# Kernel tuning notes

Measured on AMD Instinct MI355X. Metric: run time of the kernel, lower is better.

## Reference

```python
import jax, jax.numpy as jnp
import numpy as np

N_HEADS = 16
NOPE = 128
ROPE = 64
VDIM = 128
HEAD_DIM = NOPE + ROPE  # 192


def apply_rope(x, cos, sin):
    # x: [B, S, H, D] with D even; pairs (a, b) rotated by complex freqs.
    B, S, H, D = x.shape
    xr = x.reshape(B, S, H, D // 2, 2)
    a, b = xr[..., 0], xr[..., 1]
    c = cos[None, :, None, :]
    s = sin[None, :, None, :]
    out = jnp.stack([a * c - b * s, a * s + b * c], axis=-1)
    return out.reshape(B, S, H, D)


def setup_inputs() -> dict:
    key = jax.random.key(0)
    ks = jax.random.split(key, 8)
    B, S, DIM = 1, 2048, 2048
    x = jax.random.normal(ks[0], (B, S, DIM), dtype=jnp.float32)
    wq = jax.random.normal(ks[1], (N_HEADS * HEAD_DIM, DIM), dtype=jnp.float32) * (DIM ** -0.5)
    wk = jax.random.normal(ks[2], (N_HEADS * HEAD_DIM, DIM), dtype=jnp.float32) * (DIM ** -0.5)
    wv = jax.random.normal(ks[3], (N_HEADS * VDIM, DIM), dtype=jnp.float32) * (DIM ** -0.5)
    wo = jax.random.normal(ks[4], (DIM, N_HEADS * VDIM), dtype=jnp.float32) * ((N_HEADS * VDIM) ** -0.5)
    # rotary freqs: theta = 10000^{-2i/d}, angles = pos * theta
    inv_freq = 1.0 / (10000.0 ** (np.arange(0, ROPE, 2, dtype=np.float32) / ROPE))
    angles = np.arange(S, dtype=np.float32)[:, None] * inv_freq[None, :]  # [S, 32]
    freqs_cos = jnp.asarray(np.cos(angles))
    freqs_sin = jnp.asarray(np.sin(angles))
    # additive causal mask
    mask = jnp.where(jnp.triu(jnp.ones((S, S), dtype=bool), k=1), -1e9, 0.0).astype(jnp.float32)
    return {"x": x, "wq": wq, "wk": wk, "wv": wv, "wo": wo,
            "freqs_cos": freqs_cos, "freqs_sin": freqs_sin, "mask": mask, "start_pos": 0}


def reference(x, wq, wk, wv, wo, freqs_cos, freqs_sin, mask, start_pos):
    B, S, DIM = x.shape
    q = (x @ wq.T).reshape(B, S, N_HEADS, HEAD_DIM)
    k = (x @ wk.T).reshape(B, S, N_HEADS, HEAD_DIM)
    v = (x @ wv.T).reshape(B, S, N_HEADS, VDIM)
    q_nope, q_pe = q[..., :NOPE], q[..., NOPE:]
    k_nope, k_pe = k[..., :NOPE], k[..., NOPE:]
    q_pe = apply_rope(q_pe, freqs_cos, freqs_sin)
    k_pe = apply_rope(k_pe, freqs_cos, freqs_sin)
    scores = (jnp.einsum('bshd,bthd->bsht', q_nope, k_nope)
              + jnp.einsum('bshd,bthd->bsht', q_pe, k_pe)) * (HEAD_DIM ** -0.5)
    scores = scores + mask[None, :, None, :]
    probs = jax.nn.softmax(scores.astype(jnp.float32), axis=-1).astype(x.dtype)
    out = jnp.einsum('bsht,bthd->bshd', probs, v)
    return out.reshape(B, S, N_HEADS * VDIM) @ wo.T
```

## Files before the change

### kernel.cpp

```cpp
#include <hip/hip_runtime.h>
#include <hip/hip_bf16.h>
#include <math.h>

#define NH 16
#define NOPE 128
#define ROPE 64
#define VDIM 128
#define HD 192
#define SEQ 2048
#define DIM 2048
#define QKD (NH * HD)
#define VD  (NH * VDIM)
#define QKVS 8192

typedef __attribute__((ext_vector_type(8))) short short8;
typedef __attribute__((ext_vector_type(4))) short short4v;
typedef __attribute__((ext_vector_type(4))) float f32x4;
typedef unsigned int u32;

#define WAIT_VM8  0x0F78
#define WAIT_VM6  0x0F76
#define WAIT_VM4  0x0F74
#define WAIT_VM3  0x0F73
#define WAIT_VM2  0x0F72
#define WAIT_VM0  0x0F70
#define WAIT_LGKM 0xC07F

static __device__ inline short f2bf(float f) {
  union { float f; unsigned u; } v; v.f = f;
  unsigned r = (v.u + 0x7fffu + ((v.u >> 16) & 1u)) >> 16;
  return (short)r;
}
static __device__ inline float bf2f(unsigned short u) {
  union { unsigned u; float f; } v; v.u = ((unsigned)u) << 16;
  return v.f;
}

static __device__ __forceinline__ void gload16(const short* g, short* l) {
  __builtin_amdgcn_global_load_lds(
      (const __attribute__((address_space(1))) u32*)g,
      (__attribute__((address_space(3))) u32*)l, 16, 0, 0);
}


#define LSA(pp) (Lsm + (pp) * 65536)
#define LSB(pp) (Lsm + (pp) * 65536 + 32768)

#define RDA(pp, kh, mh) do { \
  const char* p_ = LSA(pp) + abase + (mh) * 8192 + ((kh) ? cx1 : cx0); \
  afr[(mh) * 4 + 0] = *(const short8*)(p_ + 0); \
  afr[(mh) * 4 + 1] = *(const short8*)(p_ + 2048); \
  afr[(mh) * 4 + 2] = *(const short8*)(p_ + 4096); \
  afr[(mh) * 4 + 3] = *(const short8*)(p_ + 6144); \
} while (0)

#define RDB(pp, kh) do { \
  const char* p_ = LSB(pp) + bbase + ((kh) ? cx1 : cx0); \
  bfr[0] = *(const short8*)(p_ + 0); \
  bfr[1] = *(const short8*)(p_ + 2048); \
  bfr[2] = *(const short8*)(p_ + 4096); \
  bfr[3] = *(const short8*)(p_ + 6144); \
} while (0)

#define SGA(kt, c) gload16(srcA[c] + (kt) * 64, (short*)(LSA((kt) & 1) + ((c) * 512 + tid) * 16))
#define SGB(kt, c) gload16(srcB[c] + (kt) * 64, (short*)(LSB((kt) & 1) + ((c) * 512 + tid) * 16))
#define G1S(kt) do { SGA(kt, 0); SGA(kt, 2); SGB(kt, 0); SGB(kt, 1); } while (0)
#define G2S(kt) do { SGA(kt, 1); SGA(kt, 3); SGB(kt, 2); SGB(kt, 3); } while (0)

#define MFMA1(mi, ni) \
  acc[mi][ni] = __builtin_amdgcn_mfma_f32_16x16x32_bf16(afr[mi], bfr[ni], acc[mi][ni], 0, 0, 0)

#define MM(mh) do { \
  MFMA1((mh)*4+0, 0); MFMA1((mh)*4+1, 0); MFMA1((mh)*4+2, 0); MFMA1((mh)*4+3, 0); \
  MFMA1((mh)*4+0, 1); MFMA1((mh)*4+1, 1); MFMA1((mh)*4+2, 1); MFMA1((mh)*4+3, 1); \
  MFMA1((mh)*4+0, 2); MFMA1((mh)*4+1, 2); MFMA1((mh)*4+2, 2); MFMA1((mh)*4+3, 2); \
  MFMA1((mh)*4+0, 3); MFMA1((mh)*4+1, 3); MFMA1((mh)*4+2, 3); MFMA1((mh)*4+3, 3); \
} while (0)

#define GBAR() __builtin_amdgcn_s_barrier()
#define GLGKM0() __builtin_amdgcn_s_waitcnt(WAIT_LGKM)
#define GPRIO1() __builtin_amdgcn_s_setprio(1)
#define GPRIO0() __builtin_amdgcn_s_setprio(0)
#define GNOP ((void)0)

#define TILE(pp, SP1, SP4, VMW) do { \
  RDA(pp, 0, 0); RDB(pp, 0); SP1; \
  GBAR(); GLGKM0(); GPRIO1(); MM(0); GPRIO0(); GBAR(); \
  RDA(pp, 0, 1); \
  GBAR(); GLGKM0(); GPRIO1(); MM(1); GPRIO0(); GBAR(); \
  RDA(pp, 1, 0); RDB(pp, 1); \
  GBAR(); GLGKM0(); GPRIO1(); MM(0); GPRIO0(); GBAR(); \
  RDA(pp, 1, 1); SP4; \
  GBAR(); GLGKM0(); GPRIO1(); MM(1); GPRIO0(); VMW; GBAR(); \
} while (0)

__global__ __launch_bounds__(512, 2) void gemm256_bt(
    const short* __restrict__ A, const short* __restrict__ B,
    short* __restrict__ C, int K, int lda, int ldb, int ldc) {
  __shared__ __align__(16) char Lsm[131072];

  const int tid = threadIdx.x;
  const int lane = tid & 63;
  const int l15 = lane & 15;
  const int quad = lane >> 4;
  const int wv = tid >> 6;
  const int wr = wv >> 2, wc = wv & 3;

  const int bid = blockIdx.x;
  const int xcd = bid & 7;
  const int idx = bid >> 3;
  const int m0 = (idx & 7) * 256;
  const int n0 = (xcd * 4 + (idx >> 3)) * 256;

  const int trow = tid >> 3;
  const int scol = ((tid & 7) * 8) ^ ((trow & 7) * 8);
  const short* srcA[4]; const short* srcB[4];
#pragma unroll
  for (int c = 0; c < 4; ++c) {
    srcA[c] = A + (size_t)(m0 + c * 64 + trow) * lda + scol;
    srcB[c] = B + (size_t)(n0 + c * 64 + trow) * ldb + scol;
  }

  const int abase = (wr * 128 + l15) * 128;
  const int bbase = (wc * 64 + l15) * 128;
  const int cx0 = (quad * 16) ^ ((l15 & 7) * 16);
  const int cx1 = (64 + quad * 16) ^ ((l15 & 7) * 16);

  f32x4 acc[8][4];
#pragma unroll
  for (int i = 0; i < 8; ++i)
#pragma unroll
    for (int j = 0; j < 4; ++j) acc[i][j] = (f32x4)(0.f);
  short8 afr[8], bfr[4];

  const int NT = K >> 6;

  G1S(0); G2S(0); G1S(1);
  __builtin_amdgcn_s_waitcnt(WAIT_VM4);
  GBAR();

  int kt = 0;
  for (; kt + 4 <= NT; kt += 2) {
    TILE(0, G2S(kt + 1), G1S(kt + 2), __builtin_amdgcn_s_waitcnt(WAIT_VM4));
    TILE(1, G2S(kt + 2), G1S(kt + 3), __builtin_amdgcn_s_waitcnt(WAIT_VM4));
  }
  TILE(0, G2S(kt + 1), GNOP, __builtin_amdgcn_s_waitcnt(WAIT_VM0));
  TILE(1, GNOP, GNOP, GNOP);

#pragma unroll
  for (int m = 0; m < 8; ++m) {
    const size_t rb = (size_t)(m0 + wr * 128 + m * 16 + quad * 4) * ldc +
                      n0 + wc * 64 + l15;
#pragma unroll
    for (int n = 0; n < 4; ++n)
#pragma unroll
      for (int r = 0; r < 4; ++r)
        C[rb + (size_t)r * ldc + n * 16] = f2bf(acc[m][n][r]);
  }
}

template <bool BF16OUT>
__global__ __launch_bounds__(256) void gemm_bt(
    const short* __restrict__ A, const short* __restrict__ B,
    void* __restrict__ Cv, int K, int lda, int ldb, int ldc, float oscale) {
  __shared__ __align__(16) short Ls[4][2][4096];

  const int tid = threadIdx.x;
  const int lane = tid & 63;
  const int wave = tid >> 6;
  const int wr = wave >> 1, wc = wave & 1;
  const int lane15 = lane & 15, quad = lane >> 4;
  const int m0 = blockIdx.y * 128, n0 = blockIdx.x * 128;

  const short* gA[4]; const short* gB[4];
#pragma unroll
  for (int i = 0; i < 4; ++i) {
    int gidx = i * 64 + lane;
    int r = gidx >> 2, p = gidx & 3;
    int g = (p ^ ((r >> 1) & 3)) * 8;
    gA[i] = A + (size_t)(m0 + wr * 64 + r) * lda + g;
    gB[i] = B + (size_t)(n0 + wc * 64 + r) * ldb + g;
  }

  f32x4 acc[4][4];
#pragma unroll
  for (int i = 0; i < 4; ++i)
#pragma unroll
    for (int j = 0; j < 4; ++j) acc[i][j] = (f32x4)(0.f);

#pragma unroll
  for (int i = 0; i < 4; ++i) gload16(gA[i], &Ls[wave][0][i * 512]);
#pragma unroll
  for (int i = 0; i < 4; ++i) gload16(gB[i], &Ls[wave][0][2048 + i * 512]);

  const int rsw = (lane15 >> 1) & 3;
  for (int k0 = 0; k0 < K; k0 += 32) {
    const int cur = (k0 >> 5) & 1;
    __builtin_amdgcn_s_waitcnt(WAIT_LGKM);
    if (k0 + 32 < K) {
      const int nxt = cur ^ 1;
#pragma unroll
      for (int i = 0; i < 4; ++i) gload16(gA[i] + k0 + 32, &Ls[wave][nxt][i * 512]);
#pragma unroll
      for (int i = 0; i < 4; ++i) gload16(gB[i] + k0 + 32, &Ls[wave][nxt][2048 + i * 512]);
      __builtin_amdgcn_s_waitcnt(WAIT_VM8);
    } else {
      __builtin_amdgcn_s_waitcnt(WAIT_VM0);
    }
    const short* bufp = &Ls[wave][cur][0];
    short8 af[4], bfv[4];
#pragma unroll
    for (int i = 0; i < 4; ++i)
      af[i] = *(const short8*)&bufp[(i * 16 + lane15) * 32 + (quad ^ rsw) * 8];
#pragma unroll
    for (int j = 0; j < 4; ++j)
      bfv[j] = *(const short8*)&bufp[2048 + (j * 16 + lane15) * 32 + (quad ^ rsw) * 8];
#pragma unroll
    for (int i = 0; i < 4; ++i)
#pragma unroll
      for (int j = 0; j < 4; ++j)
        acc[i][j] = __builtin_amdgcn_mfma_f32_16x16x32_bf16(af[i], bfv[j], acc[i][j], 0, 0, 0);
  }

#pragma unroll
  for (int i = 0; i < 4; ++i)
#pragma unroll
    for (int j = 0; j < 4; ++j)
#pragma unroll
      for (int r = 0; r < 4; ++r) {
        size_t idx = (size_t)(m0 + wr * 64 + i * 16 + quad * 4 + r) * ldc +
                     n0 + wc * 64 + j * 16 + lane15;
        if (BF16OUT)
          ((short*)Cv)[idx] = f2bf(acc[i][j][r] * oscale);
        else
          ((float*)Cv)[idx] = acc[i][j][r];
      }
}

__global__ __launch_bounds__(256) void rope_qk(
    short* __restrict__ qk, const float* __restrict__ cosf, const float* __restrict__ sinf) {
  int idx = blockIdx.x * blockDim.x + threadIdx.x;
  int j = idx & 31;
  int h = (idx >> 5) & (NH - 1);
  int s = idx >> 9;
  if (s >= SEQ) return;

  float c = cosf[s * 32 + j];
  float sn = sinf[s * 32 + j];
  size_t rowb = (size_t)s * QKVS + h * HD + NOPE + 2 * j;

  u32* pq = (u32*)(qk + rowb);
  u32 w = *pq;
  float a = bf2f((unsigned short)(w & 0xffff));
  float b = bf2f((unsigned short)(w >> 16));
  *pq = (u32)(unsigned short)f2bf(a * c - b * sn) |
        ((u32)(unsigned short)f2bf(a * sn + b * c) << 16);

  u32* pk = (u32*)(qk + rowb + QKD);
  w = *pk;
  a = bf2f((unsigned short)(w & 0xffff));
  b = bf2f((unsigned short)(w >> 16));
  *pk = (u32)(unsigned short)f2bf(a * c - b * sn) |
        ((u32)(unsigned short)f2bf(a * sn + b * c) << 16);
}

__global__ __launch_bounds__(256) void conv_in(
    const float* __restrict__ x, const float* __restrict__ wq,
    const float* __restrict__ wk, const float* __restrict__ wv,
    short* __restrict__ xb, short* __restrict__ wqkv) {
  const int NX4v = DIM * DIM / 4;
  int i = blockIdx.x * 256 + threadIdx.x;
  float4 f; short* dst; int di;
  if (i < NX4v) {
    f = ((const float4*)x)[i]; dst = xb; di = i;
  } else {
    int j = i - NX4v;
    int row = j >> 9;
    if (row < QKD) f = ((const float4*)wq)[j];
    else if (row < 2 * QKD) f = ((const float4*)wk)[j - QKD * (DIM / 4)];
    else f = ((const float4*)wv)[j - 2 * QKD * (DIM / 4)];
    dst = wqkv; di = j;
  }
  short4v o;
  o.x = f2bf(f.x); o.y = f2bf(f.y); o.z = f2bf(f.z); o.w = f2bf(f.w);
  ((short4v*)dst)[di] = o;
}

__global__ __launch_bounds__(256) void bf16_convert(
    const float* __restrict__ in, short* __restrict__ out, int n4) {
  int i = blockIdx.x * 256 + threadIdx.x;
  if (i >= n4) return;
  float4 f = ((const float4*)in)[i];
  short4v o;
  o.x = f2bf(f.x); o.y = f2bf(f.y); o.z = f2bf(f.z); o.w = f2bf(f.w);
  ((short4v*)out)[i] = o;
}

__global__ __launch_bounds__(256) void vt_bf16(
    const short* __restrict__ vb, short* __restrict__ vtb) {
  __shared__ short tile[64][74];
  const int t0 = blockIdx.x * 64;
  const int c0 = blockIdx.y * 64;
  const int tid = threadIdx.x;
#pragma unroll
  for (int i = 0; i < 16; ++i) {
    int idx = i * 256 + tid;
    int r = idx >> 6, c = idx & 63;
    tile[r][c] = vb[(size_t)(t0 + r) * QKVS + c0 + c];
  }
  __syncthreads();
  const int h = c0 >> 7;
  const int dbase = c0 & 127;
#pragma unroll
  for (int i = 0; i < 16; ++i) {
    int idx = i * 256 + tid;
    int d = idx >> 6, t = idx & 63;
    vtb[(size_t)h * VDIM * SEQ + (size_t)(dbase + d) * SEQ + t0 + t] = tile[t][d];
  }
}

#define BQ 128
#define BT 64
#define CHT 8
#define PSTR2 36
#define MFIX 8.0f

__global__ __launch_bounds__(512, 4) void attn_part(
    const short* __restrict__ qk,
    const short* __restrict__ vtb,
    short* __restrict__ Opart,
    float* __restrict__ lpart)
{
  __shared__ __align__(16) short Ks[2][BT * 192];
  __shared__ __align__(16) short Vt[VDIM * BT];
  __shared__ __align__(16) short Ps[8 * 16 * PSTR2];

  const int xcd = blockIdx.x;
  const int i0 = blockIdx.y;
  const int h = xcd + ((i0 >= 40) ? 8 : 0);
  int jj = (i0 >= 40) ? (i0 - 40) : i0;
  int qtb = 15;
  while (jj >= (qtb >> 2) + 1) { jj -= (qtb >> 2) + 1; --qtb; }
  const int chk = jj;

  const int tid = threadIdx.x;
  const int wave = tid >> 6;
  const int lane = tid & 63;
  const int lane15 = lane & 15;
  const int quad = lane >> 4;
  const int g = qtb >> 2;
  const int slot = h * 40 + (g + 1) * (2 * g + (qtb & 3)) + chk;
  const int R0 = qtb * BQ;
  const int NT = 2 * qtb + 2;
  const int kt_beg = chk * CHT;
  const int kt_end = min(kt_beg + CHT, NT);
  const float scale = 0.072168784f;

  const int qrow = R0 + wave * 16 + lane15;
  short8 qf[6];
  const short* qbase = qk + (size_t)qrow * QKVS + h * HD + quad * 8;
#pragma unroll
  for (int kc = 0; kc < 6; ++kc) qf[kc] = *(const short8*)(qbase + kc * 32);
  __builtin_amdgcn_s_waitcnt(WAIT_VM0);
  __builtin_amdgcn_sched_barrier(0);

  const short* kb = qk + QKD;
  int lKoff[3]; const short* gK[3];
#pragma unroll
  for (int i = 0; i < 3; ++i) {
    int id = i * 512 + tid;
    int row = id / 24, cX = id - row * 24;
    int ch = cX ^ (row & 7);
    lKoff[i] = id * 8;
    gK[i] = kb + (size_t)row * QKVS + h * HD + ch * 8;
  }
  const short* gV[2]; short* lV[2];
#pragma unroll
  for (int i = 0; i < 2; ++i) {
    int id = i * 512 + tid;
    int row = id >> 3, cX = id & 7;
    int ch = cX ^ (row & 7);
    lV[i] = &Vt[id * 8];
    gV[i] = vtb + (size_t)h * VDIM * SEQ + (size_t)row * SEQ + ch * 8;
  }

  f32x4 oacc[8];
#pragma unroll
  for (int i = 0; i < 8; ++i) oacc[i] = (f32x4)(0.f);
  float lsum[4] = {0.f, 0.f, 0.f, 0.f};

  short* pw = &Ps[wave * 16 * PSTR2];

  {
    const size_t t0 = (size_t)kt_beg * BT;
#pragma unroll
    for (int i = 0; i < 3; ++i) gload16(gK[i] + t0 * QKVS, &Ks[0][lKoff[i]]);
#pragma unroll
    for (int i = 0; i < 2; ++i) gload16(gV[i] + t0, lV[i]);
  }
  __builtin_amdgcn_s_waitcnt(WAIT_VM2);
  __builtin_amdgcn_s_barrier();
  __builtin_amdgcn_sched_barrier(0);

  for (int kt = kt_beg; kt < kt_end; ++kt) {
    const int cur = (kt - kt_beg) & 1;
    const bool have = (kt + 1 < kt_end);

    if (have) {
      const size_t tn = (size_t)(kt + 1) * BT;
#pragma unroll
      for (int i = 0; i < 3; ++i) gload16(gK[i] + tn * QKVS, &Ks[cur ^ 1][lKoff[i]]);
    }

    const short* kcur = &Ks[cur][0];
    f32x4 sacc[4];
    __builtin_amdgcn_s_setprio(1);
#pragma unroll
    for (int c = 0; c < 4; ++c) {
      sacc[c] = (f32x4)(0.f);
      const int row = c * 16 + lane15;
#pragma unroll
      for (int kc = 0; kc < 6; ++kc) {
        int cX = (4 * kc + quad) ^ (lane15 & 7);
        short8 kf = *(const short8*)&kcur[row * 192 + cX * 8];
        sacc[c] = __builtin_amdgcn_mfma_f32_16x16x32_bf16(qf[kc], kf, sacc[c], 0, 0, 0);
      }
    }
    __builtin_amdgcn_s_setprio(0);

    if (kt >= 2 * qtb) {
#pragma unroll
      for (int c = 0; c < 4; ++c)
#pragma unroll
        for (int r = 0; r < 4; ++r) {
          int tg = kt * BT + c * 16 + lane15;
          int qg = R0 + wave * 16 + quad * 4 + r;
          if (tg > qg) sacc[c][r] = -1e30f;
        }
    }

#pragma unroll
    for (int c = 0; c < 4; ++c)
#pragma unroll
      for (int r = 0; r < 4; ++r) {
        float p = __expf(sacc[c][r] * scale - MFIX);
        lsum[r] += p;
        sacc[c][r] = p;
      }

#pragma unroll
    for (int c = 0; c < 2; ++c)
#pragma unroll
      for (int r = 0; r < 4; ++r)
        pw[(quad * 4 + r) * PSTR2 + c * 16 + lane15] = f2bf(sacc[c][r]);
    short8 pf0 = *(const short8*)&pw[lane15 * PSTR2 + quad * 8];

    if (have) __builtin_amdgcn_s_waitcnt(WAIT_VM3);
    else      __builtin_amdgcn_s_waitcnt(WAIT_VM0);
    __builtin_amdgcn_s_barrier();
    __builtin_amdgcn_sched_barrier(0);

    __builtin_amdgcn_s_setprio(1);
#pragma unroll
    for (int ch = 0; ch < 8; ++ch) {
      const int row = ch * 16 + lane15;
      int cX0 = quad ^ (lane15 & 7);
      short8 vf0 = *(const short8*)&Vt[row * 64 + cX0 * 8];
      oacc[ch] = __builtin_amdgcn_mfma_f32_16x16x32_bf16(pf0, vf0, oacc[ch], 0, 0, 0);
    }
    __builtin_amdgcn_s_setprio(0);

#pragma unroll
    for (int c = 0; c < 2; ++c)
#pragma unroll
      for (int r = 0; r < 4; ++r)
        pw[(quad * 4 + r) * PSTR2 + c * 16 + lane15] = f2bf(sacc[2 + c][r]);
    short8 pf1 = *(const short8*)&pw[lane15 * PSTR2 + quad * 8];
    __builtin_amdgcn_s_setprio(1);
#pragma unroll
    for (int ch = 0; ch < 8; ++ch) {
      const int row = ch * 16 + lane15;
      int cX1 = (4 + quad) ^ (lane15 & 7);
      short8 vf1 = *(const short8*)&Vt[row * 64 + cX1 * 8];
      oacc[ch] = __builtin_amdgcn_mfma_f32_16x16x32_bf16(pf1, vf1, oacc[ch], 0, 0, 0);
    }
    __builtin_amdgcn_s_setprio(0);

    if (have) {
      __builtin_amdgcn_s_waitcnt(WAIT_LGKM);
      __builtin_amdgcn_s_barrier();
      const size_t tn = (size_t)(kt + 1) * BT;
#pragma unroll
      for (int i = 0; i < 2; ++i) gload16(gV[i] + tn, lV[i]);
      __builtin_amdgcn_s_waitcnt(WAIT_VM2);
      __builtin_amdgcn_s_barrier();
      __builtin_amdgcn_sched_barrier(0);
    }
  }

  short* op = Opart + (size_t)slot * (128 * 128);
#pragma unroll
  for (int ch = 0; ch < 8; ++ch)
#pragma unroll
    for (int r = 0; r < 4; ++r)
      op[(wave * 16 + quad * 4 + r) * 128 + ch * 16 + lane15] = f2bf(oacc[ch][r]);

  float red[4];
#pragma unroll
  for (int r = 0; r < 4; ++r) {
    float s = lsum[r];
    s += __shfl_xor(s, 1, 64);
    s += __shfl_xor(s, 2, 64);
    s += __shfl_xor(s, 4, 64);
    s += __shfl_xor(s, 8, 64);
    red[r] = s;
  }
  if (lane15 == 0) {
#pragma unroll
    for (int r = 0; r < 4; ++r)
      lpart[(size_t)slot * 128 + wave * 16 + quad * 4 + r] = red[r];
  }
}

__global__ __launch_bounds__(256) void attn_combine(
    const short* __restrict__ Opart, const float* __restrict__ lpart,
    short* __restrict__ aob) {
  const int qt64 = blockIdx.x, h = blockIdx.y;
  const int qtb = qt64 >> 1;
  const int half = qt64 & 1;
  const int g = qtb >> 2;
  const int nact = g + 1;
  const int base = h * 40 + (g + 1) * (2 * g + (qtb & 3));
  const int tid = threadIdx.x;
  const int row = tid >> 2;
  const int cg = (tid & 3) * 32;

  float acc[32];
#pragma unroll
  for (int e = 0; e < 32; ++e) acc[e] = 0.f;
  float lsum = 0.f;

  for (int c = 0; c < nact; ++c) {
    const short* sp = Opart + (size_t)(base + c) * (128 * 128) +
                      (half * 64 + row) * 128 + cg;
    lsum += lpart[(size_t)(base + c) * 128 + half * 64 + row];
#pragma unroll
    for (int gg = 0; gg < 4; ++gg) {
      short8 vv = *(const short8*)(sp + gg * 8);
#pragma unroll
      for (int e = 0; e < 8; ++e) acc[gg * 8 + e] += bf2f((unsigned short)vv[e]);
    }
  }

  float inv = 1.f / lsum;
#pragma unroll
  for (int gg = 0; gg < 4; ++gg) {
    short8 ov;
#pragma unroll
    for (int e = 0; e < 8; ++e) ov[e] = f2bf(acc[gg * 8 + e] * inv);
    *(short8*)(aob + (size_t)(qt64 * 64 + row) * VD + h * 128 + cg + gg * 8) = ov;
  }
}

extern "C" void kernel_launch(void* const* d_in, const int* in_sizes, int n_in,
                              void* d_out, int out_size, void* d_ws, size_t ws_size,
                              hipStream_t stream) {
  const float* x  = (const float*)d_in[0];
  const float* wq = (const float*)d_in[1];
  const float* wk = (const float*)d_in[2];
  const float* wv = (const float*)d_in[3];
  const float* wo = (const float*)d_in[4];
  const float* fc = (const float*)d_in[5];
  const float* fs = (const float*)d_in[6];

  char* ws8 = (char*)d_ws;
  short* xb    = (short*)(ws8 + 0);
  short* wo_b  = (short*)(ws8 + 0);
  short* wqkv  = (short*)(ws8 + 8388608);
  short* vtb   = (short*)(ws8 + 8388608);
  short* Opart = (short*)(ws8 + 16777216);
  float* lpart = (float*)(ws8 + 37748736);
  short* qkv   = (short*)(ws8 + 41943040);
  short* aob   = qkv;
  float* out   = (float*)d_out;

  const int NX4 = DIM * DIM / 4;
  const int NQKV4 = QKVS * DIM / 4;
  const int ROPE_GRID = (SEQ * NH * 32) / 256;

  conv_in<<<(NX4 + NQKV4) / 256, 256, 0, stream>>>(x, wq, wk, wv, xb, wqkv);

  gemm256_bt<<<dim3((QKVS / 256) * (SEQ / 256)), 512, 0, stream>>>(
      xb, wqkv, qkv, DIM, DIM, DIM, QKVS);
  rope_qk<<<ROPE_GRID, 256, 0, stream>>>(qkv, fc, fs);
  vt_bf16<<<dim3(SEQ / 64, VD / 64), 256, 0, stream>>>(qkv + 2 * QKD, vtb);

  bf16_convert<<<(NX4 + 255) / 256, 256, 0, stream>>>(wo, wo_b, NX4);

  attn_part<<<dim3(8, 80), 512, 0, stream>>>(qkv, vtb, Opart, lpart);
  attn_combine<<<dim3(SEQ / 64, NH), 256, 0, stream>>>(Opart, lpart, aob);

  gemm_bt<false><<<dim3(DIM / 128, SEQ / 128), 256, 0, stream>>>(
      aob, wo_b, out, DIM, VD, DIM, DIM, 1.0f);
}
```

Measured before the change: 312.2 us.

## Transpose QK MFMA and build P operands via lane shuffles instead of LDS

The QK^T MFMA operands are swapped so each lane holds scores for one query row across keys. The P fragments for the PV MFMA can then be assembled in registers with packed bf16 words and __shfl, rather than a round trip through an LDS scratch buffer. This removes the per-wave Ps shared array and its LDS writes and reads, and merges the two PV MFMA loops. It adds 16 shuffles per tile, which on AMD are implemented through ds_bpermute and so still use the LDS path. The row-sum reduction is simplified because of the new layout.

```diff
diff --git a/kernel.cpp b/kernel.cpp
--- a/kernel.cpp
+++ b/kernel.cpp
@@ -30,6 +30,9 @@
   union { float f; unsigned u; } v; v.f = f;
   unsigned r = (v.u + 0x7fffu + ((v.u >> 16) & 1u)) >> 16;
   return (short)r;
+}
+static __device__ inline u32 packbf(float lo, float hi) {
+  return (u32)(unsigned short)f2bf(lo) | ((u32)(unsigned short)f2bf(hi) << 16);
 }
 static __device__ inline float bf2f(unsigned short u) {
   union { unsigned u; float f; } v; v.u = ((unsigned)u) << 16;
@@ -322,7 +325,6 @@
 #define BQ 128
 #define BT 64
 #define CHT 8
-#define PSTR2 36
 #define MFIX 8.0f
 
 __global__ __launch_bounds__(512, 4) void attn_part(
@@ -333,7 +335,6 @@
 {
   __shared__ __align__(16) short Ks[2][BT * 192];
   __shared__ __align__(16) short Vt[VDIM * BT];
-  __shared__ __align__(16) short Ps[8 * 16 * PSTR2];
 
   const int xcd = blockIdx.x;
   const int i0 = blockIdx.y;
@@ -387,9 +388,11 @@
   f32x4 oacc[8];
 #pragma unroll
   for (int i = 0; i < 8; ++i) oacc[i] = (f32x4)(0.f);
-  float lsum[4] = {0.f, 0.f, 0.f, 0.f};
-
-  short* pw = &Ps[wave * 16 * PSTR2];
+  float lsum_l = 0.f;
+
+  const int sA = ((lane >> 4) & 1) * 32 + lane15;
+  const int sB = sA + 16;
+  const bool hiC = (quad >> 1) != 0;
 
   {
     const size_t t0 = (size_t)kt_beg * BT;
@@ -423,7 +426,7 @@
       for (int kc = 0; kc < 6; ++kc) {
         int cX = (4 * kc + quad) ^ (lane15 & 7);
         short8 kf = *(const short8*)&kcur[row * 192 + cX * 8];
-        sacc[c] = __builtin_amdgcn_mfma_f32_16x16x32_bf16(qf[kc], kf, sacc[c], 0, 0, 0);
+        sacc[c] = __builtin_amdgcn_mfma_f32_16x16x32_bf16(kf, qf[kc], sacc[c], 0, 0, 0);
       }
     }
     __builtin_amdgcn_s_setprio(0);
@@ -433,8 +436,8 @@
       for (int c = 0; c < 4; ++c)
 #pragma unroll
         for (int r = 0; r < 4; ++r) {
-          int tg = kt * BT + c * 16 + lane15;
-          int qg = R0 + wave * 16 + quad * 4 + r;
+          int tg = kt * BT + c * 16 + quad * 4 + r;
+          int qg = R0 + wave * 16 + lane15;
           if (tg > qg) sacc[c][r] = -1e30f;
         }
     }
@@ -444,16 +447,32 @@
 #pragma unroll
       for (int r = 0; r < 4; ++r) {
         float p = __expf(sacc[c][r] * scale - MFIX);
-        lsum[r] += p;
+        lsum_l += p;
         sacc[c][r] = p;
       }
 
-#pragma unroll
-    for (int c = 0; c < 2; ++c)
-#pragma unroll
-      for (int r = 0; r < 4; ++r)
-        pw[(quad * 4 + r) * PSTR2 + c * 16 + lane15] = f2bf(sacc[c][r]);
-    short8 pf0 = *(const short8*)&pw[lane15 * PSTR2 + quad * 8];
+    u32 w[4][2];
+#pragma unroll
+    for (int c = 0; c < 4; ++c) {
+      w[c][0] = packbf(sacc[c][0], sacc[c][1]);
+      w[c][1] = packbf(sacc[c][2], sacc[c][3]);
+    }
+
+    union { short8 s; u32 u[4]; } pf0, pf1;
+    {
+      u32 a0 = __shfl((int)w[0][0], sA), b0 = __shfl((int)w[1][0], sA);
+      u32 a1 = __shfl((int)w[0][1], sA), b1 = __shfl((int)w[1][1], sA);
+      u32 a2 = __shfl((int)w[0][0], sB), b2 = __shfl((int)w[1][0], sB);
+      u32 a3 = __shfl((int)w[0][1], sB), b3 = __shfl((int)w[1][1], sB);
+      pf0.u[0] = hiC ? b0 : a0; pf0.u[1] = hiC ? b1 : a1;
+      pf0.u[2] = hiC ? b2 : a2; pf0.u[3] = hiC ? b3 : a3;
+      u32 c0 = __shfl((int)w[2][0], sA), d0 = __shfl((int)w[3][0], sA);
+      u32 c1 = __shfl((int)w[2][1], sA), d1 = __shfl((int)w[3][1], sA);
+      u32 c2 = __shfl((int)w[2][0], sB), d2 = __shfl((int)w[3][0], sB);
+      u32 c3 = __shfl((int)w[2][1], sB), d3 = __shfl((int)w[3][1], sB);
+      pf1.u[0] = hiC ? d0 : c0; pf1.u[1] = hiC ? d1 : c1;
+      pf1.u[2] = hiC ? d2 : c2; pf1.u[3] = hiC ? d3 : c3;
+    }
 
     if (have) __builtin_amdgcn_s_waitcnt(WAIT_VM3);
     else      __builtin_amdgcn_s_waitcnt(WAIT_VM0);
@@ -465,24 +484,11 @@
     for (int ch = 0; ch < 8; ++ch) {
       const int row = ch * 16 + lane15;
       int cX0 = quad ^ (lane15 & 7);
+      int cX1 = (4 + quad) ^ (lane15 & 7);
       short8 vf0 = *(const short8*)&Vt[row * 64 + cX0 * 8];
-      oacc[ch] = __builtin_amdgcn_mfma_f32_16x16x32_bf16(pf0, vf0, oacc[ch], 0, 0, 0);
-    }
-    __builtin_amdgcn_s_setprio(0);
-
-#pragma unroll
-    for (int c = 0; c < 2; ++c)
-#pragma unroll
-      for (int r = 0; r < 4; ++r)
-        pw[(quad * 4 + r) * PSTR2 + c * 16 + lane15] = f2bf(sacc[2 + c][r]);
-    short8 pf1 = *(const short8*)&pw[lane15 * PSTR2 + quad * 8];
-    __builtin_amdgcn_s_setprio(1);
-#pragma unroll
-    for (int ch = 0; ch < 8; ++ch) {
-      const int row = ch * 16 + lane15;
-      int cX1 = (4 + quad) ^ (lane15 & 7);
       short8 vf1 = *(const short8*)&Vt[row * 64 + cX1 * 8];
-      oacc[ch] = __builtin_amdgcn_mfma_f32_16x16x32_bf16(pf1, vf1, oacc[ch], 0, 0, 0);
+      oacc[ch] = __builtin_amdgcn_mfma_f32_16x16x32_bf16(pf0.s, vf0, oacc[ch], 0, 0, 0);
+      oacc[ch] = __builtin_amdgcn_mfma_f32_16x16x32_bf16(pf1.s, vf1, oacc[ch], 0, 0, 0);
     }
     __builtin_amdgcn_s_setprio(0);
 
@@ -505,21 +511,11 @@
     for (int r = 0; r < 4; ++r)
       op[(wave * 16 + quad * 4 + r) * 128 + ch * 16 + lane15] = f2bf(oacc[ch][r]);
 
-  float red[4];
-#pragma unroll
-  for (int r = 0; r < 4; ++r) {
-    float s = lsum[r];
-    s += __shfl_xor(s, 1, 64);
-    s += __shfl_xor(s, 2, 64);
-    s += __shfl_xor(s, 4, 64);
-    s += __shfl_xor(s, 8, 64);
-    red[r] = s;
-  }
-  if (lane15 == 0) {
-#pragma unroll
-    for (int r = 0; r < 4; ++r)
-      lpart[(size_t)slot * 128 + wave * 16 + quad * 4 + r] = red[r];
-  }
+  float s = lsum_l;
+  s += __shfl_xor(s, 16, 64);
+  s += __shfl_xor(s, 32, 64);
+  if (quad == 0)
+    lpart[(size_t)slot * 128 + wave * 16 + lane15] = s;
 }
 
 __global__ __launch_bounds__(256) void attn_combine(
```

Result: no change. 311.7 us (-0.2%).
